# Optimization experiments

Hardware: AMD Instinct MI355X
Metric: run time of the kernel (lower is better)

Reference implementation:

```python
import jax, jax.numpy as jnp
import numpy as np

HIDDEN = 1024
NEG_INF = jnp.float32(-1e7)


def setup_inputs() -> dict:
    key = jax.random.key(0)
    ks = jax.random.split(key, 9)
    B, S, H = 4, 2048, HIDDEN
    std = 1.0 / np.sqrt(H)
    return {
        "queries": jax.random.normal(ks[0], (B, S, H), jnp.float32),
        "keys": jax.random.normal(ks[1], (B, S, H), jnp.float32),
        "values": jax.random.normal(ks[2], (B, S, H), jnp.float32),
        "Wq": jax.random.uniform(ks[3], (H, H), jnp.float32, -std, std),
        "bq": jax.random.uniform(ks[4], (H,), jnp.float32, -std, std),
        "Wk": jax.random.uniform(ks[5], (H, H), jnp.float32, -std, std),
        "bk": jax.random.uniform(ks[6], (H,), jnp.float32, -std, std),
        "Wv": jax.random.uniform(ks[7], (H, H), jnp.float32, -std, std),
        "bv": jax.random.uniform(ks[8], (H,), jnp.float32, -std, std),
    }


def reference(queries, keys, values, Wq, bq, Wk, bk, Wv, bv):
    # q,k,v: (B, S, H) linear projections (torch Linear: x @ W.T + b)
    q = jnp.einsum('bth,oh->bto', queries, Wq) + bq
    k = jnp.einsum('bsh,oh->bso', keys, Wk) + bk
    v = jnp.einsum('bsh,oh->bso', values, Wv) + bv
    scale = jax.lax.rsqrt(jnp.float32(q.shape[-1] * 0 + Wq.shape[0]))
    # scores[b, s, t] = <k_s, q_t> * scale   (key index s, query index t)
    scores = jnp.einsum('bsh,bth->bst', k, q) * scale
    S, T = scores.shape[1], scores.shape[2]
    # torch.tril(ones * -1e7, diagonal=-1): add -1e7 where s > t (strictly lower)
    mask = jnp.where(jnp.arange(S)[:, None] > jnp.arange(T)[None, :], NEG_INF, 0.0)
    attn = jax.nn.softmax(scores + mask, axis=1)  # softmax over key dim (dim=1)
    context = jnp.einsum('bst,bsh->bth', attn, v)  # (B, T, H)
    return context, attn
```

## Files before the change

kernel.cpp:

```cpp
#include <hip/hip_runtime.h>

typedef __bf16 bf16x8 __attribute__((ext_vector_type(8)));
typedef float f32x4 __attribute__((ext_vector_type(4)));

#define HD 1024
#define SEQ 2048
#define NB 4

__device__ inline bf16x8 load8cvt(const __bf16* p) { return *(const bf16x8*)p; }
__device__ inline bf16x8 load8cvt(const float* p) {
    f32x4 a = *(const f32x4*)p;
    f32x4 b = *(const f32x4*)(p + 4);
    bf16x8 r;
#pragma unroll
    for (int i = 0; i < 4; ++i) { r[i] = (__bf16)a[i]; r[i + 4] = (__bf16)b[i]; }
    return r;
}

__device__ inline void gld_lds16(const void* g, void* l) {
    __builtin_amdgcn_global_load_lds(
        (const __attribute__((address_space(1))) unsigned int*)g,
        (__attribute__((address_space(3))) unsigned int*)l, 16, 0, 0);
}

template <typename T>
__device__ inline void stage_tile(const T* __restrict__ G, int ld, __bf16* s, int tid)
{
    const int r  = tid >> 3;
    const int co = (tid & 7) * 8;
    if constexpr (sizeof(T) == 2) {
        __bf16* dst = s + (tid >> 6) * 512;
#pragma unroll
        for (int c = 0; c < 4; ++c)
            gld_lds16(G + (long)(c * 32 + r) * ld + co, dst + c * 2048);
    } else {
#pragma unroll
        for (int c = 0; c < 4; ++c)
            *(bf16x8*)(s + c * 2048 + tid * 8) = load8cvt(G + (long)(c * 32 + r) * ld + co);
    }
}

template <typename TA, typename TB, typename OutT,
          bool ADD_BIAS, bool STORE_VT, bool CSKIP, bool CKLIM, bool EXPSUM>
__global__ __launch_bounds__(256) void gemm_bt(
    const TA* __restrict__ A, long strideA, int lda,
    const TB* __restrict__ B, long strideB, int ldb,
    const float* __restrict__ bias,
    OutT* __restrict__ C, long strideC, int ldc,
    float* __restrict__ gsum,
    int K, float alpha)
{
    __shared__ __bf16 sA[128 * 64];
    __shared__ __bf16 sB[128 * 64];
    __shared__ float csum[128];

    const int tid = threadIdx.x;
    const int n0 = blockIdx.x * 128;
    const int m0 = blockIdx.y * 128;
    if (CSKIP && m0 > n0 + 127) return;

    const TA* Ag = A + (long)blockIdx.z * strideA + (long)m0 * lda;
    const TB* Bg = B + (long)blockIdx.z * strideB + (long)n0 * ldb;
    if (!STORE_VT) C += (long)blockIdx.z * strideC;
    if (EXPSUM) {
        gsum += (long)blockIdx.z * SEQ;
        if (tid < 128) csum[tid] = 0.f;
    }

    const int lane = tid & 63;
    const int l15  = lane & 15;
    const int quad = lane >> 4;
    const int wave = tid >> 6;
    const int wm = (wave >> 1) * 64;
    const int wn = (wave & 1) * 64;

    f32x4 acc[4][4];
    const f32x4 zero = {0.f, 0.f, 0.f, 0.f};
#pragma unroll
    for (int i = 0; i < 4; ++i)
#pragma unroll
        for (int j = 0; j < 4; ++j) acc[i][j] = zero;

    const int Kend = CKLIM ? min(K, m0 + 128) : K;

    for (int kc = 0; kc < Kend; kc += 64) {
        stage_tile(Ag + kc, lda, sA, tid);
        stage_tile(Bg + kc, ldb, sB, tid);
        __syncthreads();
#pragma unroll
        for (int kk = 0; kk < 64; kk += 32) {
            bf16x8 af[4], bf[4];
#pragma unroll
            for (int i = 0; i < 4; ++i)
                af[i] = *(const bf16x8*)&sA[(wm + i * 16 + l15) * 64 + quad * 8 + kk];
#pragma unroll
            for (int j = 0; j < 4; ++j)
                bf[j] = *(const bf16x8*)&sB[(wn + j * 16 + l15) * 64 + quad * 8 + kk];
#pragma unroll
            for (int i = 0; i < 4; ++i)
#pragma unroll
                for (int j = 0; j < 4; ++j)
                    acc[i][j] = __builtin_amdgcn_mfma_f32_16x16x32_bf16(af[i], bf[j], acc[i][j], 0, 0, 0);
        }
        __syncthreads();
    }

#pragma unroll
    for (int j = 0; j < 4; ++j) {
        const int col = n0 + wn + j * 16 + l15;
        const float bv = ADD_BIAS ? bias[col] : 0.f;
        float part = 0.f;
#pragma unroll
        for (int i = 0; i < 4; ++i) {
#pragma unroll
            for (int r = 0; r < 4; ++r) {
                const int row = m0 + wm + i * 16 + quad * 4 + r;
                float v = acc[i][j][r] * alpha + bv;
                if (EXPSUM) {
                    v = __expf(v);
                    if (row <= col) part += v;
                }
                if (STORE_VT) {
                    C[(((long)(row >> 11) * HD) + col) * SEQ + (row & (SEQ - 1))] = (OutT)v;
                } else {
                    C[(long)row * ldc + col] = (OutT)v;
                }
            }
        }
        if (EXPSUM) atomicAdd(&csum[wn + j * 16 + l15], part);
    }
    if (EXPSUM) {
        __syncthreads();
        if (tid < 128) atomicAdd(&gsum[n0 + tid], csum[tid]);
    }
}

__global__ __launch_bounds__(256) void scale_emit(
    float* __restrict__ E, const float* __restrict__ csum, __bf16* __restrict__ AT)
{
    __shared__ __bf16 tile[64][65];
    const int b = blockIdx.z;
    const int t0 = blockIdx.x * 128;
    const int s0 = blockIdx.y * 128;
    float* Eb = E + (long)b * SEQ * SEQ;
    __bf16* Ab = AT + (long)b * SEQ * SEQ;
    const int tid = threadIdx.x;

    if (s0 > t0 + 127) {
        const f32x4 z4 = {0.f, 0.f, 0.f, 0.f};
        const int c4 = (tid & 31) * 4;
        for (int r = tid >> 5; r < 128; r += 8)
            *(f32x4*)&Eb[(long)(s0 + r) * SEQ + t0 + c4] = z4;
        bf16x8 z8;
#pragma unroll
        for (int i = 0; i < 8; ++i) z8[i] = (__bf16)0.f;
        const int sc = (tid & 15) * 8;
        for (int r = tid >> 4; r < 128; r += 16)
            *(bf16x8*)&Ab[(long)(t0 + r) * SEQ + s0 + sc] = z8;
        return;
    }

#pragma unroll
    for (int ds = 0; ds < 2; ++ds) {
#pragma unroll
        for (int dt = 0; dt < 2; ++dt) {
            const int ss = s0 + ds * 64, tt = t0 + dt * 64;
            const int c4 = (tid & 15) * 4;
            const int tcol = tt + c4;
            const f32x4 sv = *(const f32x4*)&csum[(long)b * SEQ + tcol];
            f32x4 inv;
#pragma unroll
            for (int k = 0; k < 4; ++k) inv[k] = 1.0f / sv[k];
#pragma unroll
            for (int r0 = 0; r0 < 64; r0 += 16) {
                const int s = ss + r0 + (tid >> 4);
                f32x4 e = *(f32x4*)&Eb[(long)s * SEQ + tcol];
                f32x4 p;
#pragma unroll
                for (int k = 0; k < 4; ++k)
                    p[k] = (s <= tcol + k) ? e[k] * inv[k] : 0.f;
                *(f32x4*)&Eb[(long)s * SEQ + tcol] = p;
#pragma unroll
                for (int k = 0; k < 4; ++k)
                    tile[r0 + (tid >> 4)][c4 + k] = (__bf16)p[k];
            }
            __syncthreads();
            const int tr = tid >> 2;
            const int sc = (tid & 3) * 16;
            __bf16 v[16];
#pragma unroll
            for (int jj = 0; jj < 16; ++jj) v[jj] = tile[sc + jj][tr];
            *(bf16x8*)&Ab[(long)(tt + tr) * SEQ + ss + sc]     = *(bf16x8*)v;
            *(bf16x8*)&Ab[(long)(tt + tr) * SEQ + ss + sc + 8] = *(bf16x8*)(v + 8);
            __syncthreads();
        }
    }
}

__global__ __launch_bounds__(256) void cvt_bf16(
    const float* __restrict__ in, __bf16* __restrict__ out)
{
    const long i = ((long)blockIdx.x * 256 + threadIdx.x) * 8;
    *(bf16x8*)&out[i] = load8cvt(&in[i]);
}

extern "C" void kernel_launch(void* const* d_in, const int* in_sizes, int n_in,
                              void* d_out, int out_size, void* d_ws, size_t ws_size,
                              hipStream_t stream)
{
    const float* queries = (const float*)d_in[0];
    const float* keys    = (const float*)d_in[1];
    const float* values  = (const float*)d_in[2];
    const float* Wq = (const float*)d_in[3];
    const float* bq = (const float*)d_in[4];
    const float* Wk = (const float*)d_in[5];
    const float* bk = (const float*)d_in[6];
    const float* Wv = (const float*)d_in[7];
    const float* bv = (const float*)d_in[8];

    const long tokens = (long)NB * SEQ;
    const long pe = tokens * HD;

    float* outCtx  = (float*)d_out;
    float* outAttn = outCtx + tokens * HD;
    float* colsum = outCtx;

    const dim3 blk(256);
    const bool big = ws_size >= (size_t)(4 * pe * sizeof(__bf16));

    hipMemsetAsync(colsum, 0, (size_t)NB * SEQ * sizeof(float), stream);

    __bf16 *qp, *kp, *vT, *attnT;
    const dim3 gProj(HD / 128, tokens / 128, 1);

    if (big) {
        __bf16* xb = (__bf16*)d_ws;
        qp = xb + pe; kp = qp + pe; vT = kp + pe;
        attnT = (__bf16*)d_ws;
        const dim3 gCvt((unsigned)(pe / 8 / 256));

        cvt_bf16<<<gCvt, blk, 0, stream>>>(queries, xb);
        gemm_bt<__bf16, float, __bf16, true, false, false, false, false><<<gProj, blk, 0, stream>>>(
            xb, 0, HD, Wq, 0, HD, bq, qp, 0, HD, nullptr, HD, 1.0f);
        cvt_bf16<<<gCvt, blk, 0, stream>>>(keys, xb);
        gemm_bt<__bf16, float, __bf16, true, false, false, false, false><<<gProj, blk, 0, stream>>>(
            xb, 0, HD, Wk, 0, HD, bk, kp, 0, HD, nullptr, HD, 1.0f);
        cvt_bf16<<<gCvt, blk, 0, stream>>>(values, xb);
        gemm_bt<__bf16, float, __bf16, true, true, false, false, false><<<gProj, blk, 0, stream>>>(
            xb, 0, HD, Wv, 0, HD, bv, vT, 0, HD, nullptr, HD, 1.0f);
    } else {
        qp = (__bf16*)d_ws; kp = qp + pe; vT = kp + pe;
        attnT = (__bf16*)d_ws;
        gemm_bt<float, float, __bf16, true, false, false, false, false><<<gProj, blk, 0, stream>>>(
            queries, 0, HD, Wq, 0, HD, bq, qp, 0, HD, nullptr, HD, 1.0f);
        gemm_bt<float, float, __bf16, true, false, false, false, false><<<gProj, blk, 0, stream>>>(
            keys, 0, HD, Wk, 0, HD, bk, kp, 0, HD, nullptr, HD, 1.0f);
        gemm_bt<float, float, __bf16, true, true, false, false, false><<<gProj, blk, 0, stream>>>(
            values, 0, HD, Wv, 0, HD, bv, vT, 0, HD, nullptr, HD, 1.0f);
    }

    const dim3 gScores(SEQ / 128, SEQ / 128, NB);
    gemm_bt<__bf16, __bf16, float, false, false, true, false, true><<<gScores, blk, 0, stream>>>(
        kp, (long)SEQ * HD, HD, qp, (long)SEQ * HD, HD, nullptr,
        outAttn, (long)SEQ * SEQ, SEQ, colsum, HD, 0.03125f);

    scale_emit<<<dim3(SEQ / 128, SEQ / 128, NB), blk, 0, stream>>>(
        outAttn, colsum, attnT);

    const dim3 gCtx(HD / 128, SEQ / 128, NB);
    gemm_bt<__bf16, __bf16, float, false, false, false, true, false><<<gCtx, blk, 0, stream>>>(
        attnT, (long)SEQ * SEQ, SEQ, vT, (long)HD * SEQ, SEQ, nullptr,
        outCtx, (long)SEQ * HD, HD, nullptr, SEQ, 1.0f);
}
```

Before: 429.5 us.

## Batch QKV projections into one launch and use a triangular grid for scores

The three fp32-to-bf16 conversions are merged into one launch, and the three Q/K/V projection GEMMs into one launch that picks its inputs from a parameter struct indexed by blockIdx.z. When the workspace is large enough, each input gets its own buffer so all three can run concurrently. The scores GEMM now launches only the 136 upper-triangular tiles per batch, found from a linear index with a sqrt-based mapping, instead of launching the full grid and returning early. This cuts launch count and idle blocks and fills the GPU better, at the cost of more workspace and a little index arithmetic per block.

```diff
diff --git a/kernel.cpp b/kernel.cpp
--- a/kernel.cpp
+++ b/kernel.cpp
@@ -1,4 +1,5 @@
 #include <hip/hip_runtime.h>
+#include <math.h>
 
 typedef __bf16 bf16x8 __attribute__((ext_vector_type(8)));
 typedef float f32x4 __attribute__((ext_vector_type(4)));
@@ -40,32 +41,30 @@
     }
 }
 
-template <typename TA, typename TB, typename OutT,
-          bool ADD_BIAS, bool STORE_VT, bool CSKIP, bool CKLIM, bool EXPSUM>
-__global__ __launch_bounds__(256) void gemm_bt(
-    const TA* __restrict__ A, long strideA, int lda,
-    const TB* __restrict__ B, long strideB, int ldb,
-    const float* __restrict__ bias,
-    OutT* __restrict__ C, long strideC, int ldc,
-    float* __restrict__ gsum,
-    int K, float alpha)
+struct Proj3 {
+    const void* A[3];
+    const float* W[3];
+    const float* bias[3];
+    __bf16* C[3];
+    int vtmask;
+};
+
+template <typename TA>
+__global__ __launch_bounds__(256) void gemm_proj(Proj3 p)
 {
     __shared__ __bf16 sA[128 * 64];
     __shared__ __bf16 sB[128 * 64];
-    __shared__ float csum[128];
 
     const int tid = threadIdx.x;
+    const int z  = blockIdx.z;
     const int n0 = blockIdx.x * 128;
     const int m0 = blockIdx.y * 128;
-    if (CSKIP && m0 > n0 + 127) return;
-
-    const TA* Ag = A + (long)blockIdx.z * strideA + (long)m0 * lda;
-    const TB* Bg = B + (long)blockIdx.z * strideB + (long)n0 * ldb;
-    if (!STORE_VT) C += (long)blockIdx.z * strideC;
-    if (EXPSUM) {
-        gsum += (long)blockIdx.z * SEQ;
-        if (tid < 128) csum[tid] = 0.f;
-    }
+    const bool vt = (p.vtmask >> z) & 1;
+
+    const TA* Ag = (const TA*)p.A[z] + (long)m0 * HD;
+    const float* Wg = p.W[z] + (long)n0 * HD;
+    const float* bias = p.bias[z];
+    __bf16* C = p.C[z];
 
     const int lane = tid & 63;
     const int l15  = lane & 15;
@@ -81,6 +80,97 @@
 #pragma unroll
         for (int j = 0; j < 4; ++j) acc[i][j] = zero;
 
+    for (int kc = 0; kc < HD; kc += 64) {
+        stage_tile(Ag + kc, HD, sA, tid);
+        stage_tile(Wg + kc, HD, sB, tid);
+        __syncthreads();
+#pragma unroll
+        for (int kk = 0; kk < 64; kk += 32) {
+            bf16x8 af[4], bf[4];
+#pragma unroll
+            for (int i = 0; i < 4; ++i)
+                af[i] = *(const bf16x8*)&sA[(wm + i * 16 + l15) * 64 + quad * 8 + kk];
+#pragma unroll
+            for (int j = 0; j < 4; ++j)
+                bf[j] = *(const bf16x8*)&sB[(wn + j * 16 + l15) * 64 + quad * 8 + kk];
+#pragma unroll
+            for (int i = 0; i < 4; ++i)
+#pragma unroll
+                for (int j = 0; j < 4; ++j)
+                    acc[i][j] = __builtin_amdgcn_mfma_f32_16x16x32_bf16(af[i], bf[j], acc[i][j], 0, 0, 0);
+        }
+        __syncthreads();
+    }
+
+#pragma unroll
+    for (int j = 0; j < 4; ++j) {
+        const int col = n0 + wn + j * 16 + l15;
+        const float bv = bias[col];
+#pragma unroll
+        for (int i = 0; i < 4; ++i) {
+#pragma unroll
+            for (int r = 0; r < 4; ++r) {
+                const int row = m0 + wm + i * 16 + quad * 4 + r;
+                const float v = acc[i][j][r] + bv;
+                if (vt) {
+                    C[(((long)(row >> 11) * HD) + col) * SEQ + (row & (SEQ - 1))] = (__bf16)v;
+                } else {
+                    C[(long)row * HD + col] = (__bf16)v;
+                }
+            }
+        }
+    }
+}
+
+template <bool TRI, bool CKLIM, bool EXPSUM, typename OutT>
+__global__ __launch_bounds__(256) void gemm_bt(
+    const __bf16* __restrict__ A, long strideA, int lda,
+    const __bf16* __restrict__ B, long strideB, int ldb,
+    OutT* __restrict__ C, long strideC, int ldc,
+    float* __restrict__ gsum,
+    int K, float alpha)
+{
+    __shared__ __bf16 sA[128 * 64];
+    __shared__ __bf16 sB[128 * 64];
+    __shared__ float csum[128];
+
+    const int tid = threadIdx.x;
+    int n0, m0;
+    if (TRI) {
+        const int L = blockIdx.x;
+        int tb = (int)((sqrtf(8.f * L + 1.f) - 1.f) * 0.5f);
+        while ((tb + 1) * (tb + 2) / 2 <= L) ++tb;
+        while (tb * (tb + 1) / 2 > L) --tb;
+        const int sb = L - tb * (tb + 1) / 2;
+        n0 = tb * 128;
+        m0 = sb * 128;
+    } else {
+        n0 = blockIdx.x * 128;
+        m0 = blockIdx.y * 128;
+    }
+
+    const __bf16* Ag = A + (long)blockIdx.z * strideA + (long)m0 * lda;
+    const __bf16* Bg = B + (long)blockIdx.z * strideB + (long)n0 * ldb;
+    C += (long)blockIdx.z * strideC;
+    if (EXPSUM) {
+        gsum += (long)blockIdx.z * SEQ;
+        if (tid < 128) csum[tid] = 0.f;
+    }
+
+    const int lane = tid & 63;
+    const int l15  = lane & 15;
+    const int quad = lane >> 4;
+    const int wave = tid >> 6;
+    const int wm = (wave >> 1) * 64;
+    const int wn = (wave & 1) * 64;
+
+    f32x4 acc[4][4];
+    const f32x4 zero = {0.f, 0.f, 0.f, 0.f};
+#pragma unroll
+    for (int i = 0; i < 4; ++i)
+#pragma unroll
+        for (int j = 0; j < 4; ++j) acc[i][j] = zero;
+
     const int Kend = CKLIM ? min(K, m0 + 128) : K;
 
     for (int kc = 0; kc < Kend; kc += 64) {
@@ -108,23 +198,18 @@
 #pragma unroll
     for (int j = 0; j < 4; ++j) {
         const int col = n0 + wn + j * 16 + l15;
-        const float bv = ADD_BIAS ? bias[col] : 0.f;
         float part = 0.f;
 #pragma unroll
         for (int i = 0; i < 4; ++i) {
 #pragma unroll
             for (int r = 0; r < 4; ++r) {
                 const int row = m0 + wm + i * 16 + quad * 4 + r;
-                float v = acc[i][j][r] * alpha + bv;
+                float v = acc[i][j][r] * alpha;
                 if (EXPSUM) {
                     v = __expf(v);
                     if (row <= col) part += v;
                 }
-                if (STORE_VT) {
-                    C[(((long)(row >> 11) * HD) + col) * SEQ + (row & (SEQ - 1))] = (OutT)v;
-                } else {
-                    C[(long)row * ldc + col] = (OutT)v;
-                }
+                C[(long)row * ldc + col] = (OutT)v;
             }
         }
         if (EXPSUM) atomicAdd(&csum[wn + j * 16 + l15], part);
@@ -197,11 +282,12 @@
     }
 }
 
-__global__ __launch_bounds__(256) void cvt_bf16(
-    const float* __restrict__ in, __bf16* __restrict__ out)
-{
+struct Cvt3 { const float* in[3]; __bf16* out[3]; };
+__global__ __launch_bounds__(256) void cvt_bf16(Cvt3 c)
+{
+    const int z = blockIdx.y;
     const long i = ((long)blockIdx.x * 256 + threadIdx.x) * 8;
-    *(bf16x8*)&out[i] = load8cvt(&in[i]);
+    *(bf16x8*)&c.out[z][i] = load8cvt(&c.in[z][i]);
 }
 
 extern "C" void kernel_launch(void* const* d_in, const int* in_sizes, int n_in,
@@ -220,55 +306,65 @@
 
     const long tokens = (long)NB * SEQ;
     const long pe = tokens * HD;
+    const size_t SLOT = (size_t)pe * sizeof(__bf16);
 
     float* outCtx  = (float*)d_out;
     float* outAttn = outCtx + tokens * HD;
     float* colsum = outCtx;
 
     const dim3 blk(256);
-    const bool big = ws_size >= (size_t)(4 * pe * sizeof(__bf16));
-
     hipMemsetAsync(colsum, 0, (size_t)NB * SEQ * sizeof(float), stream);
 
-    __bf16 *qp, *kp, *vT, *attnT;
-    const dim3 gProj(HD / 128, tokens / 128, 1);
-
-    if (big) {
-        __bf16* xb = (__bf16*)d_ws;
-        qp = xb + pe; kp = qp + pe; vT = kp + pe;
-        attnT = (__bf16*)d_ws;
-        const dim3 gCvt((unsigned)(pe / 8 / 256));
-
-        cvt_bf16<<<gCvt, blk, 0, stream>>>(queries, xb);
-        gemm_bt<__bf16, float, __bf16, true, false, false, false, false><<<gProj, blk, 0, stream>>>(
-            xb, 0, HD, Wq, 0, HD, bq, qp, 0, HD, nullptr, HD, 1.0f);
-        cvt_bf16<<<gCvt, blk, 0, stream>>>(keys, xb);
-        gemm_bt<__bf16, float, __bf16, true, false, false, false, false><<<gProj, blk, 0, stream>>>(
-            xb, 0, HD, Wk, 0, HD, bk, kp, 0, HD, nullptr, HD, 1.0f);
-        cvt_bf16<<<gCvt, blk, 0, stream>>>(values, xb);
-        gemm_bt<__bf16, float, __bf16, true, true, false, false, false><<<gProj, blk, 0, stream>>>(
-            xb, 0, HD, Wv, 0, HD, bv, vT, 0, HD, nullptr, HD, 1.0f);
+    char* w = (char*)d_ws;
+    __bf16 *qp, *kp, *vT;
+    __bf16* attnT = (__bf16*)d_ws;
+    const dim3 gProj(HD / 128, tokens / 128, 3);
+    const unsigned nCvt = (unsigned)(pe / 8 / 256);
+
+    if (ws_size >= 6 * SLOT) {
+        __bf16* xq = (__bf16*)w;
+        __bf16* xk = (__bf16*)(w + SLOT);
+        __bf16* xv = (__bf16*)(w + 2 * SLOT);
+        qp = (__bf16*)(w + 3 * SLOT);
+        kp = (__bf16*)(w + 4 * SLOT);
+        vT = (__bf16*)(w + 5 * SLOT);
+        Cvt3 cv = {{queries, keys, values}, {xq, xk, xv}};
+        cvt_bf16<<<dim3(nCvt, 3), blk, 0, stream>>>(cv);
+        Proj3 pj = {{xq, xk, xv}, {Wq, Wk, Wv}, {bq, bk, bv}, {qp, kp, vT}, 4};
+        gemm_proj<__bf16><<<gProj, blk, 0, stream>>>(pj);
+    } else if (ws_size >= 4 * SLOT) {
+        __bf16* x0 = (__bf16*)w;
+        qp = (__bf16*)(w + SLOT);
+        kp = (__bf16*)(w + 2 * SLOT);
+        __bf16* x1 = (__bf16*)(w + 3 * SLOT);
+        vT = x1;
+        Cvt3 cv = {{queries, keys, nullptr}, {x0, x1, nullptr}};
+        cvt_bf16<<<dim3(nCvt, 2), blk, 0, stream>>>(cv);
+        Proj3 pqk = {{x0, x1, nullptr}, {Wq, Wk, nullptr}, {bq, bk, nullptr},
+                     {qp, kp, nullptr}, 0};
+        gemm_proj<__bf16><<<dim3(HD / 128, tokens / 128, 2), blk, 0, stream>>>(pqk);
+        Cvt3 cvv = {{values, nullptr, nullptr}, {x0, nullptr, nullptr}};
+        cvt_bf16<<<dim3(nCvt, 1), blk, 0, stream>>>(cvv);
+        Proj3 pv = {{x0, nullptr, nullptr}, {Wv, nullptr, nullptr},
+                    {bv, nullptr, nullptr}, {vT, nullptr, nullptr}, 1};
+        gemm_proj<__bf16><<<dim3(HD / 128, tokens / 128, 1), blk, 0, stream>>>(pv);
     } else {
-        qp = (__bf16*)d_ws; kp = qp + pe; vT = kp + pe;
-        attnT = (__bf16*)d_ws;
-        gemm_bt<float, float, __bf16, true, false, false, false, false><<<gProj, blk, 0, stream>>>(
-            queries, 0, HD, Wq, 0, HD, bq, qp, 0, HD, nullptr, HD, 1.0f);
-        gemm_bt<float, float, __bf16, true, false, false, false, false><<<gProj, blk, 0, stream>>>(
-            keys, 0, HD, Wk, 0, HD, bk, kp, 0, HD, nullptr, HD, 1.0f);
-        gemm_bt<float, float, __bf16, true, true, false, false, false><<<gProj, blk, 0, stream>>>(
-            values, 0, HD, Wv, 0, HD, bv, vT, 0, HD, nullptr, HD, 1.0f);
-    }
-
-    const dim3 gScores(SEQ / 128, SEQ / 128, NB);
-    gemm_bt<__bf16, __bf16, float, false, false, true, false, true><<<gScores, blk, 0, stream>>>(
-        kp, (long)SEQ * HD, HD, qp, (long)SEQ * HD, HD, nullptr,
+        qp = (__bf16*)w;
+        kp = (__bf16*)(w + SLOT);
+        vT = (__bf16*)(w + 2 * SLOT);
+        Proj3 pj = {{queries, keys, values}, {Wq, Wk, Wv}, {bq, bk, bv},
+                    {qp, kp, vT}, 4};
+        gemm_proj<float><<<gProj, blk, 0, stream>>>(pj);
+    }
+
+    gemm_bt<true, false, true, float><<<dim3(136, 1, NB), blk, 0, stream>>>(
+        kp, (long)SEQ * HD, HD, qp, (long)SEQ * HD, HD,
         outAttn, (long)SEQ * SEQ, SEQ, colsum, HD, 0.03125f);
 
     scale_emit<<<dim3(SEQ / 128, SEQ / 128, NB), blk, 0, stream>>>(
         outAttn, colsum, attnT);
 
-    const dim3 gCtx(HD / 128, SEQ / 128, NB);
-    gemm_bt<__bf16, __bf16, float, false, false, false, true, false><<<gCtx, blk, 0, stream>>>(
-        attnT, (long)SEQ * SEQ, SEQ, vT, (long)HD * SEQ, SEQ, nullptr,
+    gemm_bt<false, true, false, float><<<dim3(HD / 128, SEQ / 128, NB), blk, 0, stream>>>(
+        attnT, (long)SEQ * SEQ, SEQ, vT, (long)HD * SEQ, SEQ,
         outCtx, (long)SEQ * HD, HD, nullptr, SEQ, 1.0f);
 }
```

Measured after the change: 415.6 us. -3.2%, faster.
